# Kernel tuning notes

Hardware: AMD Instinct MI355X
Metric: run time of the kernel (lower is better)

Reference implementation:

```python
import jax, jax.numpy as jnp
import numpy as np

B, T, IN = 64, 366, 24
H1, H2, HM, PEN, C = 1024, 2048, 2048, 1024, 21


def setup_inputs() -> dict:
    key = jax.random.key(0)
    ks = jax.random.split(key, 20)
    s = 0.02
    inp = {
        'x': jax.random.normal(ks[0], (B, T, IN), jnp.float32),
        'cultivar_label': jax.random.randint(ks[1], (B, 1), 0, C, jnp.int64),
        'W1': jax.random.normal(ks[2], (H1, IN), jnp.float32) * s,
        'b1': jnp.zeros((H1,), jnp.float32),
        'W2': jax.random.normal(ks[3], (H2, H1), jnp.float32) * s,
        'b2': jnp.zeros((H2,), jnp.float32),
        'W_ih': jax.random.normal(ks[4], (3 * HM, H2), jnp.float32) * s,
        'W_hh': jax.random.normal(ks[5], (3 * HM, HM), jnp.float32) * s,
        'b_ih': jnp.zeros((3 * HM,), jnp.float32),
        'b_hh': jnp.zeros((3 * HM,), jnp.float32),
        'W3': jax.random.normal(ks[6], (PEN, HM), jnp.float32) * s,
        'b3': jnp.zeros((PEN,), jnp.float32),
        'W4': jax.random.normal(ks[7], (C, PEN), jnp.float32) * s,
        'b4': jnp.zeros((C,), jnp.float32),
        'W5': jax.random.normal(ks[8], (C, PEN), jnp.float32) * s,
        'b5': jnp.zeros((C,), jnp.float32),
        'W6': jax.random.normal(ks[9], (C, PEN), jnp.float32) * s,
        'b6': jnp.zeros((C,), jnp.float32),
    }
    return inp


def _gru(x_btd, W_ih, W_hh, b_ih, b_hh):
    # PyTorch GRU, gate order (r, z, n). x_btd: [B,T,H2]
    xg = jnp.einsum('btd,gd->btg', x_btd, W_ih) + b_ih  # [B,T,3*HM]
    h0 = jnp.zeros((x_btd.shape[0], HM), x_btd.dtype)

    def step(h, xg_t):
        hg = h @ W_hh.T + b_hh
        xr, xz, xn = jnp.split(xg_t, 3, axis=-1)
        hr, hz, hn = jnp.split(hg, 3, axis=-1)
        r = jax.nn.sigmoid(xr + hr)
        z = jax.nn.sigmoid(xz + hz)
        n = jnp.tanh(xn + r * hn)
        h_new = (1.0 - z) * n + z * h
        return h_new, h_new

    h_last, hs = jax.lax.scan(step, h0, jnp.swapaxes(xg, 0, 1))
    return jnp.swapaxes(hs, 0, 1), h_last  # [B,T,HM], [B,HM]


def reference(x, cultivar_label, W1, b1, W2, b2, W_ih, W_hh, b_ih, b_hh,
              W3, b3, W4, b4, W5, b5, W6, b6):
    out = jax.nn.relu(jnp.einsum('bti,oi->bto', x, W1) + b1)
    out = jax.nn.relu(jnp.einsum('bti,oi->bto', out, W2) + b2)
    out, h_next = _gru(out, W_ih, W_hh, b_ih, b_hh)
    out_s = jax.nn.relu(jnp.einsum('bti,oi->bto', out, W3) + b3)  # [B,T,PEN]
    labels = cultivar_label[:, 0]  # [B]

    def head(W, b):
        w = W[labels]            # [B,PEN] gathered per-sample head weights
        bb = b[labels]           # [B]
        y = jnp.einsum('btp,bp->bt', out_s, w) + bb[:, None]
        return y[..., None]      # [B,T,1]

    return head(W4, b4), head(W5, b5), head(W6, b6), 0, 0
```

## Files before the change

kernel.cpp:

```cpp
#include <hip/hip_runtime.h>
#include <math.h>

#define B_   64
#define T_   366
#define IN_  24
#define H1_  1024
#define H2_  2048
#define HM_  2048
#define G3_  (3 * HM_)
#define PEN_ 1024
#define C_   21
#define BT_  (B_ * T_)

#define TC_  61
#define NCH  6
#define MC   (B_ * TC_)

typedef unsigned short bf16_t;
typedef __bf16 bf16x8 __attribute__((ext_vector_type(8)));
typedef float  f32x4  __attribute__((ext_vector_type(4)));

__device__ __forceinline__ float bf2f(bf16_t u) {
  return __uint_as_float(((unsigned int)u) << 16);
}
__device__ __forceinline__ bf16_t f2bf(float f) {
  unsigned int x = __float_as_uint(f);
  unsigned int r = (x + 0x7fffu + ((x >> 16) & 1u)) >> 16;
  return (bf16_t)r;
}

struct ushort4_t { bf16_t x, y, z, w; };

#define GBM 128
#define GBN 128
#define GBK 32
#define LDT 40

template<int WBF>
__global__ __launch_bounds__(256) void gemm_mfma(
    const bf16_t* __restrict__ A, const float* __restrict__ Wf,
    const bf16_t* __restrict__ Wb,
    const float* __restrict__ bias, bf16_t* __restrict__ C,
    int M, int N, int K, int relu)
{
  __shared__ bf16_t Asl[GBM * LDT];
  __shared__ bf16_t Wsl[GBN * LDT];
  const int tid  = threadIdx.x;
  const int m0   = blockIdx.x * GBM;
  const int n0   = blockIdx.y * GBN;
  const int wave = tid >> 6;
  const int lane = tid & 63;
  const int l16  = lane & 15;
  const int quad = lane >> 4;
  const int wm   = (wave & 1) * 64;
  const int wn   = (wave >> 1) * 64;
  const int srow = tid >> 1;
  const int sseg = (tid & 1) << 4;
  const int arow = (m0 + srow < M) ? (m0 + srow) : (M - 1);

  f32x4 acc[4][4];
  #pragma unroll
  for (int i = 0; i < 4; ++i)
    #pragma unroll
    for (int j = 0; j < 4; ++j)
      acc[i][j] = (f32x4){0.f, 0.f, 0.f, 0.f};

  for (int k0 = 0; k0 < K; k0 += GBK) {
    {
      const bf16_t* ga = A + (size_t)arow * K + k0 + sseg;
      const uint4 a0 = *(const uint4*)ga;
      const uint4 a1 = *(const uint4*)(ga + 8);
      *(uint4*)&Asl[srow * LDT + sseg]     = a0;
      *(uint4*)&Asl[srow * LDT + sseg + 8] = a1;
      if (WBF) {
        const bf16_t* gw = Wb + (size_t)(n0 + srow) * K + k0 + sseg;
        const uint4 w0 = *(const uint4*)gw;
        const uint4 w1 = *(const uint4*)(gw + 8);
        *(uint4*)&Wsl[srow * LDT + sseg]     = w0;
        *(uint4*)&Wsl[srow * LDT + sseg + 8] = w1;
      } else {
        const float* gw = Wf + (size_t)(n0 + srow) * K + k0 + sseg;
        const float4 w0 = *(const float4*)gw;
        const float4 w1 = *(const float4*)(gw + 4);
        const float4 w2 = *(const float4*)(gw + 8);
        const float4 w3 = *(const float4*)(gw + 12);
        ushort4_t p0 = {f2bf(w0.x), f2bf(w0.y), f2bf(w0.z), f2bf(w0.w)};
        ushort4_t p1 = {f2bf(w1.x), f2bf(w1.y), f2bf(w1.z), f2bf(w1.w)};
        ushort4_t p2 = {f2bf(w2.x), f2bf(w2.y), f2bf(w2.z), f2bf(w2.w)};
        ushort4_t p3 = {f2bf(w3.x), f2bf(w3.y), f2bf(w3.z), f2bf(w3.w)};
        *(ushort4_t*)&Wsl[srow * LDT + sseg]      = p0;
        *(ushort4_t*)&Wsl[srow * LDT + sseg + 4]  = p1;
        *(ushort4_t*)&Wsl[srow * LDT + sseg + 8]  = p2;
        *(ushort4_t*)&Wsl[srow * LDT + sseg + 12] = p3;
      }
    }
    __syncthreads();
    bf16x8 af[4], bf[4];
    #pragma unroll
    for (int i = 0; i < 4; ++i)
      af[i] = *(const bf16x8*)&Asl[(wm + 16 * i + l16) * LDT + quad * 8];
    #pragma unroll
    for (int j = 0; j < 4; ++j)
      bf[j] = *(const bf16x8*)&Wsl[(wn + 16 * j + l16) * LDT + quad * 8];
    #pragma unroll
    for (int i = 0; i < 4; ++i)
      #pragma unroll
      for (int j = 0; j < 4; ++j)
        acc[i][j] = __builtin_amdgcn_mfma_f32_16x16x32_bf16(af[i], bf[j], acc[i][j], 0, 0, 0);
    __syncthreads();
  }

  #pragma unroll
  for (int j = 0; j < 4; ++j) {
    const int n = n0 + wn + 16 * j + l16;
    const float bn = bias[n];
    #pragma unroll
    for (int i = 0; i < 4; ++i) {
      #pragma unroll
      for (int reg = 0; reg < 4; ++reg) {
        const int m = m0 + wm + 16 * i + quad * 4 + reg;
        if (m < M) {
          float v = acc[i][j][reg] + bn;
          if (relu) v = fmaxf(v, 0.f);
          C[(size_t)m * N + n] = f2bf(v);
        }
      }
    }
  }
}

#define HLD 72

__global__ __launch_bounds__(512) void gru_step(
    const bf16_t* __restrict__ h_bf_in, float* __restrict__ h_f,
    const bf16_t* __restrict__ Whh_bf, const bf16_t* __restrict__ xg_c,
    const float* __restrict__ b_hh,
    bf16_t* __restrict__ h_bf_out, bf16_t* __restrict__ hs_c, int tt)
{
  __shared__ bf16_t hst[2][64 * HLD];
  __shared__ bf16_t wst[2][48 * HLD];
  const int tid  = threadIdx.x;
  const int team = tid >> 8;
  const int ttid = tid & 255;
  const int wave = (tid >> 6) & 3;
  const int lane = tid & 63;
  const int l16  = lane & 15;
  const int quad = lane >> 4;
  const int j0   = blockIdx.x * 16;
  const int j    = j0 + l16;

  f32x4 acc[3];
  acc[0] = (f32x4){0.f, 0.f, 0.f, 0.f};
  acc[1] = acc[0];
  acc[2] = acc[0];

  const int hrow = ttid >> 2;
  const int hseg = (ttid & 3) << 4;
  const int wg   = hrow >> 4;
  const int wjr  = hrow & 15;
  const int kbase = team * (HM_ / 2);

  const bf16_t* gh_base = h_bf_in + (size_t)hrow * HM_ + kbase + hseg;
  const bf16_t* gw_base = Whh_bf + (size_t)(wg * HM_ + j0 + wjr) * HM_ + kbase + hseg;

  bf16_t xrb[4], xzb[4], xnb[4];
  float  hp[4];
  if (team == 0) {
    #pragma unroll
    for (int reg = 0; reg < 4; ++reg) {
      const int b = wave * 16 + quad * 4 + reg;
      const size_t xrow = (size_t)(b * TC_ + tt) * G3_;
      xrb[reg] = xg_c[xrow + j];
      xzb[reg] = xg_c[xrow + HM_ + j];
      xnb[reg] = xg_c[xrow + 2 * HM_ + j];
      hp[reg]  = h_f[b * HM_ + j];
    }
  }

  uint4 h0 = *(const uint4*)(gh_base);
  uint4 h1 = *(const uint4*)(gh_base + 8);
  uint4 w0 = {0u,0u,0u,0u}, w1 = {0u,0u,0u,0u};
  if (ttid < 192) { w0 = *(const uint4*)(gw_base); w1 = *(const uint4*)(gw_base + 8); }

  for (int k0 = 0; k0 < HM_ / 2; k0 += 64) {
    *(uint4*)&hst[team][hrow * HLD + hseg]     = h0;
    *(uint4*)&hst[team][hrow * HLD + hseg + 8] = h1;
    if (ttid < 192) {
      *(uint4*)&wst[team][hrow * HLD + hseg]     = w0;
      *(uint4*)&wst[team][hrow * HLD + hseg + 8] = w1;
    }
    __syncthreads();
    if (k0 + 64 < HM_ / 2) {
      h0 = *(const uint4*)(gh_base + k0 + 64);
      h1 = *(const uint4*)(gh_base + k0 + 64 + 8);
      if (ttid < 192) {
        w0 = *(const uint4*)(gw_base + k0 + 64);
        w1 = *(const uint4*)(gw_base + k0 + 64 + 8);
      }
    }
    #pragma unroll
    for (int s = 0; s < 2; ++s) {
      const bf16x8 afr = *(const bf16x8*)&hst[team][(wave * 16 + l16) * HLD + s * 32 + quad * 8];
      #pragma unroll
      for (int g = 0; g < 3; ++g) {
        const bf16x8 bfr = *(const bf16x8*)&wst[team][(g * 16 + l16) * HLD + s * 32 + quad * 8];
        acc[g] = __builtin_amdgcn_mfma_f32_16x16x32_bf16(afr, bfr, acc[g], 0, 0, 0);
      }
    }
    __syncthreads();
  }

  float* red = (float*)&hst[0][0];
  if (team == 1) {
    #pragma unroll
    for (int g = 0; g < 3; ++g)
      #pragma unroll
      for (int r = 0; r < 4; ++r)
        red[ttid * 12 + g * 4 + r] = acc[g][r];
  }
  __syncthreads();
  if (team == 1) return;
  #pragma unroll
  for (int g = 0; g < 3; ++g)
    #pragma unroll
    for (int r = 0; r < 4; ++r)
      acc[g][r] += red[ttid * 12 + g * 4 + r];

  const float bh_r = b_hh[j];
  const float bh_z = b_hh[HM_ + j];
  const float bh_n = b_hh[2 * HM_ + j];
  #pragma unroll
  for (int reg = 0; reg < 4; ++reg) {
    const int b = wave * 16 + quad * 4 + reg;
    const float xr = bf2f(xrb[reg]);
    const float xz = bf2f(xzb[reg]);
    const float xn = bf2f(xnb[reg]);
    const float r = 1.f / (1.f + expf(-(xr + acc[0][reg] + bh_r)));
    const float z = 1.f / (1.f + expf(-(xz + acc[1][reg] + bh_z)));
    const float n = tanhf(xn + r * (acc[2][reg] + bh_n));
    const float hnew = (1.f - z) * n + z * hp[reg];
    h_f[b * HM_ + j] = hnew;
    const bf16_t hb = f2bf(hnew);
    h_bf_out[b * HM_ + j] = hb;
    hs_c[(size_t)(b * TC_ + tt) * HM_ + j] = hb;
  }
}

#define BM 64
#define BN 64
#define BKK 16

__global__ __launch_bounds__(256) void gemm_l1_gather(
    const float* __restrict__ x, const float* __restrict__ W,
    const float* __restrict__ bias, bf16_t* __restrict__ C, int t0)
{
  __shared__ float As[BKK][BM];
  __shared__ float Ws[BKK][BN];
  const int tid = threadIdx.x;
  const int m0 = blockIdx.x * BM;
  const int n0 = blockIdx.y * BN;
  const int lr = tid >> 2;
  const int kq = (tid & 3) << 2;
  const int ty = tid >> 4;
  const int tx = tid & 15;
  const int r = m0 + lr;
  const int b = r / TC_;
  const int tt = r - b * TC_;
  const size_t srow = (size_t)b * T_ + t0 + tt;
  float acc[4][4] = {};
  for (int k0 = 0; k0 < IN_; k0 += BKK) {
    {
      float v0 = 0.f, v1 = 0.f, v2 = 0.f, v3 = 0.f;
      const int kk = k0 + kq;
      const float* src = x + srow * IN_ + kk;
      if (kk + 4 <= IN_) {
        const float4 v = *(const float4*)src;
        v0 = v.x; v1 = v.y; v2 = v.z; v3 = v.w;
      }
      As[kq + 0][lr] = v0; As[kq + 1][lr] = v1;
      As[kq + 2][lr] = v2; As[kq + 3][lr] = v3;
      float w0 = 0.f, w1 = 0.f, w2 = 0.f, w3 = 0.f;
      const float* srcw = W + (size_t)(n0 + lr) * IN_ + kk;
      if (kk + 4 <= IN_) {
        const float4 w = *(const float4*)srcw;
        w0 = w.x; w1 = w.y; w2 = w.z; w3 = w.w;
      }
      Ws[kq + 0][lr] = w0; Ws[kq + 1][lr] = w1;
      Ws[kq + 2][lr] = w2; Ws[kq + 3][lr] = w3;
    }
    __syncthreads();
    #pragma unroll
    for (int k = 0; k < BKK; ++k) {
      const float4 av = *(const float4*)&As[k][ty << 2];
      const float4 bv = *(const float4*)&Ws[k][tx << 2];
      const float aa[4] = {av.x, av.y, av.z, av.w};
      const float bb[4] = {bv.x, bv.y, bv.z, bv.w};
      #pragma unroll
      for (int i = 0; i < 4; ++i)
        #pragma unroll
        for (int j = 0; j < 4; ++j)
          acc[i][j] = fmaf(aa[i], bb[j], acc[i][j]);
    }
    __syncthreads();
  }
  const float4 bvec = *(const float4*)&bias[n0 + (tx << 2)];
  const float bb[4] = {bvec.x, bvec.y, bvec.z, bvec.w};
  #pragma unroll
  for (int i = 0; i < 4; ++i) {
    ushort4_t ov;
    ov.x = f2bf(fmaxf(acc[i][0] + bb[0], 0.f));
    ov.y = f2bf(fmaxf(acc[i][1] + bb[1], 0.f));
    ov.z = f2bf(fmaxf(acc[i][2] + bb[2], 0.f));
    ov.w = f2bf(fmaxf(acc[i][3] + bb[3], 0.f));
    *(ushort4_t*)&C[(size_t)(m0 + (ty << 2) + i) * H1_ + n0 + (tx << 2)] = ov;
  }
}

__global__ __launch_bounds__(256) void heads_kernel(
    const bf16_t* __restrict__ outs_c, const int* __restrict__ label,
    const float* __restrict__ W4, const float* __restrict__ b4,
    const float* __restrict__ W5, const float* __restrict__ b5,
    const float* __restrict__ W6, const float* __restrict__ b6,
    float* __restrict__ out, int t0)
{
  const int r = blockIdx.x;
  const int b = r / TC_;
  const int tt = r - b * TC_;
  int lab = label[b];
  lab = lab < 0 ? 0 : (lab > C_ - 1 ? C_ - 1 : lab);
  const int tid = threadIdx.x;
  const bf16_t* o = outs_c + (size_t)r * PEN_;
  const float* w4 = W4 + (size_t)lab * PEN_;
  const float* w5 = W5 + (size_t)lab * PEN_;
  const float* w6 = W6 + (size_t)lab * PEN_;
  float s4 = 0.f, s5 = 0.f, s6 = 0.f;
  for (int p = tid; p < PEN_; p += 256) {
    const float ov = bf2f(o[p]);
    s4 = fmaf(ov, w4[p], s4);
    s5 = fmaf(ov, w5[p], s5);
    s6 = fmaf(ov, w6[p], s6);
  }
  #pragma unroll
  for (int off = 32; off > 0; off >>= 1) {
    s4 += __shfl_down(s4, off, 64);
    s5 += __shfl_down(s5, off, 64);
    s6 += __shfl_down(s6, off, 64);
  }
  __shared__ float red[4][3];
  const int wave = tid >> 6;
  if ((tid & 63) == 0) { red[wave][0] = s4; red[wave][1] = s5; red[wave][2] = s6; }
  __syncthreads();
  if (tid == 0) {
    const int bt = b * T_ + t0 + tt;
    out[bt]           = red[0][0] + red[1][0] + red[2][0] + red[3][0] + b4[lab];
    out[BT_ + bt]     = red[0][1] + red[1][1] + red[2][1] + red[3][1] + b5[lab];
    out[2 * BT_ + bt] = red[0][2] + red[1][2] + red[2][2] + red[3][2] + b6[lab];
    if (t0 == 0 && r == 0) { out[3 * BT_] = 0.f; out[3 * BT_ + 1] = 0.f; }
  }
}

__global__ __launch_bounds__(256) void cvt_bf(const float* __restrict__ src,
                                              bf16_t* __restrict__ dst, int n) {
  const int i = (blockIdx.x * 256 + threadIdx.x) * 4;
  if (i + 4 <= n) {
    const float4 v = *(const float4*)&src[i];
    ushort4_t o = {f2bf(v.x), f2bf(v.y), f2bf(v.z), f2bf(v.w)};
    *(ushort4_t*)&dst[i] = o;
  }
}

__global__ __launch_bounds__(256) void zero_h(float* __restrict__ hf,
                                              bf16_t* __restrict__ hb0,
                                              bf16_t* __restrict__ hb1) {
  const int i = blockIdx.x * 256 + threadIdx.x;
  hf[i] = 0.f; hb0[i] = 0; hb1[i] = 0;
}

extern "C" void kernel_launch(void* const* d_in, const int* in_sizes, int n_in,
                              void* d_out, int out_size, void* d_ws, size_t ws_size,
                              hipStream_t stream) {
  const float* x     = (const float*)d_in[0];
  const int*   label = (const int*)d_in[1];
  const float* W1    = (const float*)d_in[2];
  const float* b1    = (const float*)d_in[3];
  const float* W2    = (const float*)d_in[4];
  const float* b2    = (const float*)d_in[5];
  const float* W_ih  = (const float*)d_in[6];
  const float* W_hh  = (const float*)d_in[7];
  const float* b_ih  = (const float*)d_in[8];
  const float* b_hh  = (const float*)d_in[9];
  const float* W3    = (const float*)d_in[10];
  const float* b3    = (const float*)d_in[11];
  const float* W4    = (const float*)d_in[12];
  const float* b4    = (const float*)d_in[13];
  const float* W5    = (const float*)d_in[14];
  const float* b5    = (const float*)d_in[15];
  const float* W6    = (const float*)d_in[16];
  const float* b6    = (const float*)d_in[17];

  const size_t NEEDED  = 98172928UL;
  const size_t NEEDED2 = 131727360UL;
  if (ws_size < NEEDED) return;
  const int use_bf = (ws_size >= NEEDED2);

  char* ws = (char*)d_ws;
  bf16_t* xg_c   = (bf16_t*)(ws + 0);
  bf16_t* out2_c = (bf16_t*)(ws + 47972352UL);
  bf16_t* hs_c   = out2_c;
  bf16_t* out1_c = (bf16_t*)(ws + 63963136UL);
  bf16_t* outs_c = out1_c;
  bf16_t* Whh_bf = (bf16_t*)(ws + 71958528UL);
  float*  h_f    = (float*)(ws + 97124352UL);
  bf16_t* hbuf[2];
  hbuf[0] = (bf16_t*)(ws + 97648640UL);
  hbuf[1] = (bf16_t*)(ws + 97910784UL);
  bf16_t* W2b  = (bf16_t*)(ws + 98172928UL);
  bf16_t* Wihb = (bf16_t*)(ws + 102367232UL);
  bf16_t* W3b  = (bf16_t*)(ws + 127533056UL);
  float* out = (float*)d_out;

  const dim3 blk(256);

  cvt_bf<<<dim3(G3_ * HM_ / 1024), blk, 0, stream>>>(W_hh, Whh_bf, G3_ * HM_);
  zero_h<<<dim3(B_ * HM_ / 256), blk, 0, stream>>>(h_f, hbuf[0], hbuf[1]);
  if (use_bf) {
    cvt_bf<<<dim3(H2_ * H1_ / 1024), blk, 0, stream>>>(W2, W2b, H2_ * H1_);
    cvt_bf<<<dim3(G3_ * H2_ / 1024), blk, 0, stream>>>(W_ih, Wihb, G3_ * H2_);
    cvt_bf<<<dim3(PEN_ * HM_ / 1024), blk, 0, stream>>>(W3, W3b, PEN_ * HM_);
  }

  int pp = 0;
  for (int c = 0; c < NCH; ++c) {
    const int t0 = c * TC_;
    gemm_l1_gather<<<dim3(MC / BM, H1_ / BN), blk, 0, stream>>>(x, W1, b1, out1_c, t0);
    if (use_bf) {
      gemm_mfma<1><<<dim3((MC + GBM - 1) / GBM, H2_ / GBN), blk, 0, stream>>>(
          out1_c, nullptr, W2b, b2, out2_c, MC, H2_, H1_, 1);
      gemm_mfma<1><<<dim3((MC + GBM - 1) / GBM, G3_ / GBN), blk, 0, stream>>>(
          out2_c, nullptr, Wihb, b_ih, xg_c, MC, G3_, H2_, 0);
    } else {
      gemm_mfma<0><<<dim3((MC + GBM - 1) / GBM, H2_ / GBN), blk, 0, stream>>>(
          out1_c, W2, nullptr, b2, out2_c, MC, H2_, H1_, 1);
      gemm_mfma<0><<<dim3((MC + GBM - 1) / GBM, G3_ / GBN), blk, 0, stream>>>(
          out2_c, W_ih, nullptr, b_ih, xg_c, MC, G3_, H2_, 0);
    }

    for (int tt = 0; tt < TC_; ++tt) {
      gru_step<<<dim3(HM_ / 16), dim3(512), 0, stream>>>(
          hbuf[pp], h_f, Whh_bf, xg_c, b_hh, hbuf[1 - pp], hs_c, tt);
      pp ^= 1;
    }

    if (use_bf) {
      gemm_mfma<1><<<dim3((MC + GBM - 1) / GBM, PEN_ / GBN), blk, 0, stream>>>(
          hs_c, nullptr, W3b, b3, outs_c, MC, PEN_, HM_, 1);
    } else {
      gemm_mfma<0><<<dim3((MC + GBM - 1) / GBM, PEN_ / GBN), blk, 0, stream>>>(
          hs_c, W3, nullptr, b3, outs_c, MC, PEN_, HM_, 1);
    }
    heads_kernel<<<dim3(MC), blk, 0, stream>>>(
        outs_c, label, W4, b4, W5, b5, W6, b6, out, t0);
  }
}
```

Measured before the change: 6.947 ms.

## Fuse GRU timesteps into persistent cooperative kernel with LDS-resident W_hh slices

Replaces the per-timestep gru_step launches with one cooperative kernel per chunk of 61 timesteps. Each of 256 blocks keeps its 24-row slice of W_hh in LDS for the whole chunk and synchronises across the grid between steps. This is meant to remove hundreds of launches and the repeated reloading of W_hh on every step, at the cost of a grid-wide barrier per step. Separately, the bf16 GEMM path now copies global tiles straight into unpadded LDS with global_load_lds, which skips the register round-trip but may add LDS bank conflicts. If the cooperative launch fails, the code falls back to the old per-step kernel.

```diff
diff --git a/kernel.cpp b/kernel.cpp
--- a/kernel.cpp
+++ b/kernel.cpp
@@ -1,4 +1,5 @@
 #include <hip/hip_runtime.h>
+#include <hip/hip_cooperative_groups.h>
 #include <math.h>
 
 #define B_   64
@@ -30,6 +31,9 @@
 }
 
 struct ushort4_t { bf16_t x, y, z, w; };
+
+#define AS1 __attribute__((address_space(1)))
+#define AS3 __attribute__((address_space(3)))
 
 #define GBM 128
 #define GBN 128
@@ -54,9 +58,6 @@
   const int quad = lane >> 4;
   const int wm   = (wave & 1) * 64;
   const int wn   = (wave >> 1) * 64;
-  const int srow = tid >> 1;
-  const int sseg = (tid & 1) << 4;
-  const int arow = (m0 + srow < M) ? (m0 + srow) : (M - 1);
 
   f32x4 acc[4][4];
   #pragma unroll
@@ -65,20 +66,47 @@
     for (int j = 0; j < 4; ++j)
       acc[i][j] = (f32x4){0.f, 0.f, 0.f, 0.f};
 
-  for (int k0 = 0; k0 < K; k0 += GBK) {
-    {
-      const bf16_t* ga = A + (size_t)arow * K + k0 + sseg;
-      const uint4 a0 = *(const uint4*)ga;
-      const uint4 a1 = *(const uint4*)(ga + 8);
-      *(uint4*)&Asl[srow * LDT + sseg]     = a0;
-      *(uint4*)&Asl[srow * LDT + sseg + 8] = a1;
-      if (WBF) {
-        const bf16_t* gw = Wb + (size_t)(n0 + srow) * K + k0 + sseg;
-        const uint4 w0 = *(const uint4*)gw;
-        const uint4 w1 = *(const uint4*)(gw + 8);
-        *(uint4*)&Wsl[srow * LDT + sseg]     = w0;
-        *(uint4*)&Wsl[srow * LDT + sseg + 8] = w1;
-      } else {
+  if (WBF) {
+    const int r4 = lane >> 2;
+    const int sg = (lane & 3) << 3;
+    for (int k0 = 0; k0 < K; k0 += GBK) {
+      #pragma unroll
+      for (int it = 0; it < 2; ++it) {
+        const int row = wave * 32 + it * 16 + r4;
+        const int ar  = (m0 + row < M) ? (m0 + row) : (M - 1);
+        __builtin_amdgcn_global_load_lds(
+            (const AS1 void*)(A + (size_t)ar * K + k0 + sg),
+            (AS3 void*)&Asl[(wave * 2 + it) * 512], 16, 0, 0);
+        __builtin_amdgcn_global_load_lds(
+            (const AS1 void*)(Wb + (size_t)(n0 + row) * K + k0 + sg),
+            (AS3 void*)&Wsl[(wave * 2 + it) * 512], 16, 0, 0);
+      }
+      __syncthreads();
+      bf16x8 af[4], bfr[4];
+      #pragma unroll
+      for (int i = 0; i < 4; ++i)
+        af[i] = *(const bf16x8*)&Asl[(wm + 16 * i + l16) * 32 + quad * 8];
+      #pragma unroll
+      for (int j = 0; j < 4; ++j)
+        bfr[j] = *(const bf16x8*)&Wsl[(wn + 16 * j + l16) * 32 + quad * 8];
+      #pragma unroll
+      for (int i = 0; i < 4; ++i)
+        #pragma unroll
+        for (int j = 0; j < 4; ++j)
+          acc[i][j] = __builtin_amdgcn_mfma_f32_16x16x32_bf16(af[i], bfr[j], acc[i][j], 0, 0, 0);
+      __syncthreads();
+    }
+  } else {
+    const int srow = tid >> 1;
+    const int sseg = (tid & 1) << 4;
+    const int arow = (m0 + srow < M) ? (m0 + srow) : (M - 1);
+    for (int k0 = 0; k0 < K; k0 += GBK) {
+      {
+        const bf16_t* ga = A + (size_t)arow * K + k0 + sseg;
+        const uint4 a0 = *(const uint4*)ga;
+        const uint4 a1 = *(const uint4*)(ga + 8);
+        *(uint4*)&Asl[srow * LDT + sseg]     = a0;
+        *(uint4*)&Asl[srow * LDT + sseg + 8] = a1;
         const float* gw = Wf + (size_t)(n0 + srow) * K + k0 + sseg;
         const float4 w0 = *(const float4*)gw;
         const float4 w1 = *(const float4*)(gw + 4);
@@ -93,21 +121,21 @@
         *(ushort4_t*)&Wsl[srow * LDT + sseg + 8]  = p2;
         *(ushort4_t*)&Wsl[srow * LDT + sseg + 12] = p3;
       }
-    }
-    __syncthreads();
-    bf16x8 af[4], bf[4];
-    #pragma unroll
-    for (int i = 0; i < 4; ++i)
-      af[i] = *(const bf16x8*)&Asl[(wm + 16 * i + l16) * LDT + quad * 8];
-    #pragma unroll
-    for (int j = 0; j < 4; ++j)
-      bf[j] = *(const bf16x8*)&Wsl[(wn + 16 * j + l16) * LDT + quad * 8];
-    #pragma unroll
-    for (int i = 0; i < 4; ++i)
+      __syncthreads();
+      bf16x8 af[4], bfr[4];
+      #pragma unroll
+      for (int i = 0; i < 4; ++i)
+        af[i] = *(const bf16x8*)&Asl[(wm + 16 * i + l16) * LDT + quad * 8];
       #pragma unroll
       for (int j = 0; j < 4; ++j)
-        acc[i][j] = __builtin_amdgcn_mfma_f32_16x16x32_bf16(af[i], bf[j], acc[i][j], 0, 0, 0);
-    __syncthreads();
+        bfr[j] = *(const bf16x8*)&Wsl[(wn + 16 * j + l16) * LDT + quad * 8];
+      #pragma unroll
+      for (int i = 0; i < 4; ++i)
+        #pragma unroll
+        for (int j = 0; j < 4; ++j)
+          acc[i][j] = __builtin_amdgcn_mfma_f32_16x16x32_bf16(af[i], bfr[j], acc[i][j], 0, 0, 0);
+      __syncthreads();
+    }
   }
 
   #pragma unroll
@@ -130,6 +158,127 @@
 }
 
 #define HLD 72
+#define WLDP 2056
+
+__global__ __launch_bounds__(512) void gru_chunk(
+    float* __restrict__ h_f,
+    const bf16_t* __restrict__ Whh_bf, const bf16_t* __restrict__ xg_c,
+    const float* __restrict__ b_hh,
+    bf16_t* __restrict__ hb0, bf16_t* __restrict__ hb1,
+    bf16_t* __restrict__ hs_c, int pp0)
+{
+  __shared__ bf16_t wlds[24 * WLDP];
+  __shared__ bf16_t hst[2][64 * HLD];
+  const int tid   = threadIdx.x;
+  const int team  = tid >> 8;
+  const int ttid  = tid & 255;
+  const int wave4 = ttid >> 6;
+  const int lane  = tid & 63;
+  const int l16   = lane & 15;
+  const int quad  = lane >> 4;
+  const int j0    = blockIdx.x * 8;
+  const int kbase = team * (HM_ / 2);
+
+  for (int idx = tid; idx < 24 * 256; idx += 512) {
+    const int r   = idx >> 8;
+    const int c16 = idx & 255;
+    const int g   = r >> 3;
+    const int jj  = j0 + (r & 7);
+    const uint4 v = *(const uint4*)(Whh_bf + (size_t)(g * HM_ + jj) * HM_ + c16 * 8);
+    *(uint4*)&wlds[r * WLDP + c16 * 8] = v;
+  }
+
+  const int ej  = tid & 7;
+  const int eb  = tid >> 3;
+  const int jje = j0 + ej;
+  const float bhr = b_hh[jje];
+  const float bhz = b_hh[HM_ + jje];
+  const float bhn = b_hh[2 * HM_ + jje];
+
+  const int hrow = ttid >> 2;
+  const int hseg = (ttid & 3) << 4;
+
+  bf16_t* hb[2] = {hb0, hb1};
+  float* red = (float*)&hst[0][0];
+  #define RIDX(t,g,j,b) ((((t)*3+(g))*8+(j))*65 + (b))
+
+  __syncthreads();
+
+  for (int tt = 0; tt < TC_; ++tt) {
+    const bf16_t* hin  = hb[(pp0 + tt) & 1];
+    bf16_t*       hout = hb[(pp0 + tt + 1) & 1];
+    const bf16_t* gh_base = hin + (size_t)hrow * HM_ + kbase + hseg;
+
+    const size_t xrow = (size_t)(eb * TC_ + tt) * G3_;
+    const bf16_t xrb = xg_c[xrow + jje];
+    const bf16_t xzb = xg_c[xrow + HM_ + jje];
+    const bf16_t xnb = xg_c[xrow + 2 * HM_ + jje];
+    const float  hp  = h_f[eb * HM_ + jje];
+
+    uint4 a0 = *(const uint4*)(gh_base);
+    uint4 a1 = *(const uint4*)(gh_base + 8);
+    uint4 c0 = *(const uint4*)(gh_base + 64);
+    uint4 c1 = *(const uint4*)(gh_base + 64 + 8);
+
+    f32x4 acc0 = (f32x4){0.f, 0.f, 0.f, 0.f};
+    f32x4 acc1 = acc0;
+
+    for (int k0 = 0; k0 < HM_ / 2; k0 += 64) {
+      *(uint4*)&hst[team][hrow * HLD + hseg]     = a0;
+      *(uint4*)&hst[team][hrow * HLD + hseg + 8] = a1;
+      __syncthreads();
+      a0 = c0; a1 = c1;
+      if (k0 + 128 < HM_ / 2) {
+        c0 = *(const uint4*)(gh_base + k0 + 128);
+        c1 = *(const uint4*)(gh_base + k0 + 128 + 8);
+      }
+      #pragma unroll
+      for (int s = 0; s < 2; ++s) {
+        const bf16x8 afr = *(const bf16x8*)&hst[team][(wave4 * 16 + l16) * HLD + s * 32 + quad * 8];
+        const int kw = kbase + k0 + s * 32 + quad * 8;
+        const bf16x8 b0 = *(const bf16x8*)&wlds[l16 * WLDP + kw];
+        const bf16x8 b1 = *(const bf16x8*)&wlds[(16 + (l16 & 7)) * WLDP + kw];
+        acc0 = __builtin_amdgcn_mfma_f32_16x16x32_bf16(afr, b0, acc0, 0, 0, 0);
+        acc1 = __builtin_amdgcn_mfma_f32_16x16x32_bf16(afr, b1, acc1, 0, 0, 0);
+      }
+      __syncthreads();
+    }
+
+    {
+      const int g0  = (l16 < 8) ? 0 : 1;
+      const int jj0 = l16 & 7;
+      #pragma unroll
+      for (int reg = 0; reg < 4; ++reg) {
+        const int b = wave4 * 16 + quad * 4 + reg;
+        red[RIDX(team, g0, jj0, b)] = acc0[reg];
+      }
+      if (l16 < 8) {
+        #pragma unroll
+        for (int reg = 0; reg < 4; ++reg) {
+          const int b = wave4 * 16 + quad * 4 + reg;
+          red[RIDX(team, 2, l16, b)] = acc1[reg];
+        }
+      }
+    }
+    __syncthreads();
+
+    {
+      const float sr = red[RIDX(0, 0, ej, eb)] + red[RIDX(1, 0, ej, eb)];
+      const float sz = red[RIDX(0, 1, ej, eb)] + red[RIDX(1, 1, ej, eb)];
+      const float sn = red[RIDX(0, 2, ej, eb)] + red[RIDX(1, 2, ej, eb)];
+      const float xr = bf2f(xrb), xz = bf2f(xzb), xn = bf2f(xnb);
+      const float r = 1.f / (1.f + expf(-(xr + sr + bhr)));
+      const float z = 1.f / (1.f + expf(-(xz + sz + bhz)));
+      const float n = tanhf(xn + r * (sn + bhn));
+      const float hnew = (1.f - z) * n + z * hp;
+      h_f[eb * HM_ + jje] = hnew;
+      const bf16_t hbv = f2bf(hnew);
+      hout[eb * HM_ + jje] = hbv;
+      hs_c[(size_t)(eb * TC_ + tt) * HM_ + jje] = hbv;
+    }
+    cooperative_groups::this_grid().sync();
+  }
+}
 
 __global__ __launch_bounds__(512) void gru_step(
     const bf16_t* __restrict__ h_bf_in, float* __restrict__ h_f,
@@ -430,6 +579,7 @@
   }
 
   int pp = 0;
+  int coop_ok = 1;
   for (int c = 0; c < NCH; ++c) {
     const int t0 = c * TC_;
     gemm_l1_gather<<<dim3(MC / BM, H1_ / BN), blk, 0, stream>>>(x, W1, b1, out1_c, t0);
@@ -445,10 +595,24 @@
           out2_c, W_ih, nullptr, b_ih, xg_c, MC, G3_, H2_, 0);
     }
 
-    for (int tt = 0; tt < TC_; ++tt) {
-      gru_step<<<dim3(HM_ / 16), dim3(512), 0, stream>>>(
-          hbuf[pp], h_f, Whh_bf, xg_c, b_hh, hbuf[1 - pp], hs_c, tt);
-      pp ^= 1;
+    if (coop_ok) {
+      float* hf_ = h_f; const bf16_t* whh_ = Whh_bf; const bf16_t* xgp_ = xg_c;
+      const float* bhh_ = b_hh; bf16_t* h0_ = hbuf[0]; bf16_t* h1_ = hbuf[1];
+      bf16_t* hs_ = hs_c; int pp_ = pp;
+      void* args[8] = {&hf_, &whh_, &xgp_, &bhh_, &h0_, &h1_, &hs_, &pp_};
+      if (hipLaunchCooperativeKernel((const void*)gru_chunk, dim3(256), dim3(512),
+                                     args, 0, stream) == hipSuccess) {
+        pp ^= 1;
+      } else {
+        coop_ok = 0;
+      }
+    }
+    if (!coop_ok) {
+      for (int tt = 0; tt < TC_; ++tt) {
+        gru_step<<<dim3(HM_ / 16), dim3(512), 0, stream>>>(
+            hbuf[pp], h_f, Whh_bf, xg_c, b_hh, hbuf[1 - pp], hs_c, tt);
+        pp ^= 1;
+      }
     }
 
     if (use_bf) {
```

Result: slower. 16.46 ms (+137.0%).

## Use direct global-to-LDS loads in bf16 GEMM and double-buffer GRU step tiles

Applied to the files above, without the earlier changes.

In the bf16-weight GEMM path, tiles now go straight from global memory into LDS through the global_load_lds builtin with an unpadded 32-wide layout, instead of being staged through registers. In the GRU recurrent step, the LDS tiles are double-buffered, so each chunk needs one barrier instead of two and the next chunk's loads overlap the current MFMAs. The unpadded GEMM LDS layout may bring bank conflicts, and the doubled GRU LDS footprint may reduce occupancy.

```diff
diff --git a/kernel.cpp b/kernel.cpp
--- a/kernel.cpp
+++ b/kernel.cpp
@@ -30,6 +30,9 @@
 }
 
 struct ushort4_t { bf16_t x, y, z, w; };
+
+#define AS1 __attribute__((address_space(1)))
+#define AS3 __attribute__((address_space(3)))
 
 #define GBM 128
 #define GBN 128
@@ -54,9 +57,6 @@
   const int quad = lane >> 4;
   const int wm   = (wave & 1) * 64;
   const int wn   = (wave >> 1) * 64;
-  const int srow = tid >> 1;
-  const int sseg = (tid & 1) << 4;
-  const int arow = (m0 + srow < M) ? (m0 + srow) : (M - 1);
 
   f32x4 acc[4][4];
   #pragma unroll
@@ -65,20 +65,47 @@
     for (int j = 0; j < 4; ++j)
       acc[i][j] = (f32x4){0.f, 0.f, 0.f, 0.f};
 
-  for (int k0 = 0; k0 < K; k0 += GBK) {
-    {
-      const bf16_t* ga = A + (size_t)arow * K + k0 + sseg;
-      const uint4 a0 = *(const uint4*)ga;
-      const uint4 a1 = *(const uint4*)(ga + 8);
-      *(uint4*)&Asl[srow * LDT + sseg]     = a0;
-      *(uint4*)&Asl[srow * LDT + sseg + 8] = a1;
-      if (WBF) {
-        const bf16_t* gw = Wb + (size_t)(n0 + srow) * K + k0 + sseg;
-        const uint4 w0 = *(const uint4*)gw;
-        const uint4 w1 = *(const uint4*)(gw + 8);
-        *(uint4*)&Wsl[srow * LDT + sseg]     = w0;
-        *(uint4*)&Wsl[srow * LDT + sseg + 8] = w1;
-      } else {
+  if (WBF) {
+    const int r4 = lane >> 2;
+    const int sg = (lane & 3) << 3;
+    for (int k0 = 0; k0 < K; k0 += GBK) {
+      #pragma unroll
+      for (int it = 0; it < 2; ++it) {
+        const int row = wave * 32 + it * 16 + r4;
+        const int ar  = (m0 + row < M) ? (m0 + row) : (M - 1);
+        __builtin_amdgcn_global_load_lds(
+            (const AS1 void*)(A + (size_t)ar * K + k0 + sg),
+            (AS3 void*)&Asl[(wave * 2 + it) * 512], 16, 0, 0);
+        __builtin_amdgcn_global_load_lds(
+            (const AS1 void*)(Wb + (size_t)(n0 + row) * K + k0 + sg),
+            (AS3 void*)&Wsl[(wave * 2 + it) * 512], 16, 0, 0);
+      }
+      __syncthreads();
+      bf16x8 af[4], bfr[4];
+      #pragma unroll
+      for (int i = 0; i < 4; ++i)
+        af[i] = *(const bf16x8*)&Asl[(wm + 16 * i + l16) * 32 + quad * 8];
+      #pragma unroll
+      for (int j = 0; j < 4; ++j)
+        bfr[j] = *(const bf16x8*)&Wsl[(wn + 16 * j + l16) * 32 + quad * 8];
+      #pragma unroll
+      for (int i = 0; i < 4; ++i)
+        #pragma unroll
+        for (int j = 0; j < 4; ++j)
+          acc[i][j] = __builtin_amdgcn_mfma_f32_16x16x32_bf16(af[i], bfr[j], acc[i][j], 0, 0, 0);
+      __syncthreads();
+    }
+  } else {
+    const int srow = tid >> 1;
+    const int sseg = (tid & 1) << 4;
+    const int arow = (m0 + srow < M) ? (m0 + srow) : (M - 1);
+    for (int k0 = 0; k0 < K; k0 += GBK) {
+      {
+        const bf16_t* ga = A + (size_t)arow * K + k0 + sseg;
+        const uint4 a0 = *(const uint4*)ga;
+        const uint4 a1 = *(const uint4*)(ga + 8);
+        *(uint4*)&Asl[srow * LDT + sseg]     = a0;
+        *(uint4*)&Asl[srow * LDT + sseg + 8] = a1;
         const float* gw = Wf + (size_t)(n0 + srow) * K + k0 + sseg;
         const float4 w0 = *(const float4*)gw;
         const float4 w1 = *(const float4*)(gw + 4);
@@ -93,21 +120,21 @@
         *(ushort4_t*)&Wsl[srow * LDT + sseg + 8]  = p2;
         *(ushort4_t*)&Wsl[srow * LDT + sseg + 12] = p3;
       }
-    }
-    __syncthreads();
-    bf16x8 af[4], bf[4];
-    #pragma unroll
-    for (int i = 0; i < 4; ++i)
-      af[i] = *(const bf16x8*)&Asl[(wm + 16 * i + l16) * LDT + quad * 8];
-    #pragma unroll
-    for (int j = 0; j < 4; ++j)
-      bf[j] = *(const bf16x8*)&Wsl[(wn + 16 * j + l16) * LDT + quad * 8];
-    #pragma unroll
-    for (int i = 0; i < 4; ++i)
+      __syncthreads();
+      bf16x8 af[4], bfr[4];
+      #pragma unroll
+      for (int i = 0; i < 4; ++i)
+        af[i] = *(const bf16x8*)&Asl[(wm + 16 * i + l16) * LDT + quad * 8];
       #pragma unroll
       for (int j = 0; j < 4; ++j)
-        acc[i][j] = __builtin_amdgcn_mfma_f32_16x16x32_bf16(af[i], bf[j], acc[i][j], 0, 0, 0);
-    __syncthreads();
+        bfr[j] = *(const bf16x8*)&Wsl[(wn + 16 * j + l16) * LDT + quad * 8];
+      #pragma unroll
+      for (int i = 0; i < 4; ++i)
+        #pragma unroll
+        for (int j = 0; j < 4; ++j)
+          acc[i][j] = __builtin_amdgcn_mfma_f32_16x16x32_bf16(af[i], bfr[j], acc[i][j], 0, 0, 0);
+      __syncthreads();
+    }
   }
 
   #pragma unroll
@@ -137,8 +164,8 @@
     const float* __restrict__ b_hh,
     bf16_t* __restrict__ h_bf_out, bf16_t* __restrict__ hs_c, int tt)
 {
-  __shared__ bf16_t hst[2][64 * HLD];
-  __shared__ bf16_t wst[2][48 * HLD];
+  __shared__ bf16_t hst[2][2][64 * HLD];
+  __shared__ bf16_t wst[2][2][48 * HLD];
   const int tid  = threadIdx.x;
   const int team = tid >> 8;
   const int ttid = tid & 255;
@@ -177,40 +204,54 @@
     }
   }
 
-  uint4 h0 = *(const uint4*)(gh_base);
-  uint4 h1 = *(const uint4*)(gh_base + 8);
-  uint4 w0 = {0u,0u,0u,0u}, w1 = {0u,0u,0u,0u};
-  if (ttid < 192) { w0 = *(const uint4*)(gw_base); w1 = *(const uint4*)(gw_base + 8); }
-
+  {
+    uint4 h0 = *(const uint4*)(gh_base);
+    uint4 h1 = *(const uint4*)(gh_base + 8);
+    *(uint4*)&hst[team][0][hrow * HLD + hseg]     = h0;
+    *(uint4*)&hst[team][0][hrow * HLD + hseg + 8] = h1;
+    if (ttid < 192) {
+      uint4 w0 = *(const uint4*)(gw_base);
+      uint4 w1 = *(const uint4*)(gw_base + 8);
+      *(uint4*)&wst[team][0][hrow * HLD + hseg]     = w0;
+      *(uint4*)&wst[team][0][hrow * HLD + hseg + 8] = w1;
+    }
+  }
+  __syncthreads();
+
+  int cur = 0;
   for (int k0 = 0; k0 < HM_ / 2; k0 += 64) {
-    *(uint4*)&hst[team][hrow * HLD + hseg]     = h0;
-    *(uint4*)&hst[team][hrow * HLD + hseg + 8] = h1;
-    if (ttid < 192) {
-      *(uint4*)&wst[team][hrow * HLD + hseg]     = w0;
-      *(uint4*)&wst[team][hrow * HLD + hseg + 8] = w1;
+    uint4 nh0, nh1, nw0, nw1;
+    const int have_next = (k0 + 64 < HM_ / 2);
+    if (have_next) {
+      nh0 = *(const uint4*)(gh_base + k0 + 64);
+      nh1 = *(const uint4*)(gh_base + k0 + 64 + 8);
+      if (ttid < 192) {
+        nw0 = *(const uint4*)(gw_base + k0 + 64);
+        nw1 = *(const uint4*)(gw_base + k0 + 64 + 8);
+      }
+    }
+    #pragma unroll
+    for (int s = 0; s < 2; ++s) {
+      const bf16x8 afr = *(const bf16x8*)&hst[team][cur][(wave * 16 + l16) * HLD + s * 32 + quad * 8];
+      #pragma unroll
+      for (int g = 0; g < 3; ++g) {
+        const bf16x8 bfr = *(const bf16x8*)&wst[team][cur][(g * 16 + l16) * HLD + s * 32 + quad * 8];
+        acc[g] = __builtin_amdgcn_mfma_f32_16x16x32_bf16(afr, bfr, acc[g], 0, 0, 0);
+      }
+    }
+    if (have_next) {
+      *(uint4*)&hst[team][cur ^ 1][hrow * HLD + hseg]     = nh0;
+      *(uint4*)&hst[team][cur ^ 1][hrow * HLD + hseg + 8] = nh1;
+      if (ttid < 192) {
+        *(uint4*)&wst[team][cur ^ 1][hrow * HLD + hseg]     = nw0;
+        *(uint4*)&wst[team][cur ^ 1][hrow * HLD + hseg + 8] = nw1;
+      }
     }
     __syncthreads();
-    if (k0 + 64 < HM_ / 2) {
-      h0 = *(const uint4*)(gh_base + k0 + 64);
-      h1 = *(const uint4*)(gh_base + k0 + 64 + 8);
-      if (ttid < 192) {
-        w0 = *(const uint4*)(gw_base + k0 + 64);
-        w1 = *(const uint4*)(gw_base + k0 + 64 + 8);
-      }
-    }
-    #pragma unroll
-    for (int s = 0; s < 2; ++s) {
-      const bf16x8 afr = *(const bf16x8*)&hst[team][(wave * 16 + l16) * HLD + s * 32 + quad * 8];
-      #pragma unroll
-      for (int g = 0; g < 3; ++g) {
-        const bf16x8 bfr = *(const bf16x8*)&wst[team][(g * 16 + l16) * HLD + s * 32 + quad * 8];
-        acc[g] = __builtin_amdgcn_mfma_f32_16x16x32_bf16(afr, bfr, acc[g], 0, 0, 0);
-      }
-    }
-    __syncthreads();
-  }
-
-  float* red = (float*)&hst[0][0];
+    cur ^= 1;
+  }
+
+  float* red = (float*)&hst[0][0][0];
   if (team == 1) {
     #pragma unroll
     for (int g = 0; g < 3; ++g)
```

New measurement: 6.945 ms. Within noise of the previous version (-0.0%).
